# Performance work log

Hardware: AMD Instinct MI355X
Metric: run time of the kernel (lower is better)

Reference implementation:

```python
import jax, jax.numpy as jnp
import numpy as np

# --- config-derived constants (match init_kwargs) ---
BATCH = 16
TEMP = 0.1
N_REGIONS = 9
IMG = 512
NUM_FILTERS = 5      # len(no_filters)-1
N_DEC_BLOCKS = 2
SIZE_FACTOR = 1 << (NUM_FILTERS - N_DEC_BLOCKS)   # 8
IM = IMG // SIZE_FACTOR - 4                        # 60
H = W = IM + 2                                     # 62 (feature map spatial size)
C = 512
EPS = 1e-6

_h = IM // 2  # 30
_X = _Y = IM  # 60
POS = np.array([[0,0],[0,_h],[0,_Y],[_h,0],[_h,_h],[_h,_Y],[_X,0],[_X,_h],[_X,_Y]], np.int32)
NEG = np.array([
  [[0,_h],[_h,0],[_h,_h],[0,_Y],[_X,0]],
  [[0,0],[0,_Y],[_h,0],[_h,_h],[_h,_Y]],
  [[0,0],[0,_h],[_h,_h],[_h,_Y],[_X,_Y]],
  [[0,0],[0,_h],[_h,_h],[_X,0],[_X,_h]],
  [[0,0],[0,_h],[_h,0],[_h,_Y],[_X,_h]],
  [[0,_h],[0,_Y],[_h,_h],[_X,_h],[_X,_Y]],
  [[0,0],[_h,0],[_h,_h],[_X,_h],[_X,_Y]],
  [[_h,0],[_h,_h],[_h,_Y],[_X,0],[_X,_Y]],
  [[0,_Y],[_h,_h],[_h,_Y],[_X,0],[_X,_h]],
], np.int32)

def _patch_flat(idx):
    # idx [..., 2] (row, col) -> flat indices of the 2x2 patch, [..., 4]
    base = idx[..., 0] * W + idx[..., 1]
    return np.stack([base, base + 1, base + W, base + W + 1], axis=-1)

POS_FLAT = jnp.asarray(_patch_flat(POS))     # [9, 4]
NEG_FLAT = jnp.asarray(_patch_flat(NEG))     # [9, 5, 4]

def _cos(a, b):
    # cosine similarity over last axis, torch-style eps clamp on the norm product
    dot = jnp.sum(a * b, axis=-1)
    na = jnp.sqrt(jnp.sum(a * a, axis=-1))
    nb = jnp.sqrt(jnp.sum(b * b, axis=-1))
    return dot / jnp.maximum(na * nb, EPS)


def setup_inputs() -> dict:
    key = jax.random.key(0)
    x = jax.random.normal(key, (BATCH, C, H, W), dtype=jnp.float32)
    return {"x": x}


def reference(x):
    B = x.shape[0]
    xf = x.reshape(B, C, H * W)
    pp = xf[:, :, POS_FLAT]   # [B, C, 9, 4]
    nn_ = xf[:, :, NEG_FLAT]  # [B, C, 9, 5, 4]
    i1p, i2p = pp[0::2], pp[1::2]      # [P, C, 9, 4]
    i1n, i2n = nn_[0::2], nn_[1::2]    # [P, C, 9, 5, 4]

    # positive similarity (symmetric: cos(i1,i2) == cos(i2,i1))
    num_ss = _cos(i1p, i2p) / TEMP                 # [P, C, 9]
    S = jnp.sum(jnp.exp(num_ss), axis=1)           # [P, 9]

    a1 = i1p[:, :, :, None, :]                     # [P, C, 9, 1, 4]
    a2 = i2p[:, :, :, None, :]
    den1 = jnp.exp(_cos(a1, i1n) / TEMP) + jnp.exp(_cos(a1, i2n) / TEMP)  # [P, C, 9, 5]
    den2 = jnp.exp(_cos(a2, i2n) / TEMP) + jnp.exp(_cos(a2, i1n) / TEMP)
    D1 = jnp.sum(den1, axis=(1, 3))                # [P, 9]
    D2 = jnp.sum(den2, axis=(1, 3))

    loss = jnp.sum(-jnp.log(S / (S + D1)) - jnp.log(S / (S + D2)))
    return loss / B / N_REGIONS
```

## Files before the change

### kernel.cpp

```cpp
#include <hip/hip_runtime.h>
#include <math.h>

#define NPAIR 8
#define NREG 9
#define NCH 512
#define HW 3844
#define W62 62
#define NPATCH 9

__constant__ int PATCH_BASE[9] = {0, 30, 60, 1860, 1890, 1920, 3720, 3750, 3780};
__constant__ int NEG_IDX[9][5] = {
    {1, 3, 4, 2, 6},
    {0, 2, 3, 4, 5},
    {0, 1, 4, 5, 8},
    {0, 1, 4, 6, 7},
    {0, 1, 3, 5, 7},
    {1, 2, 4, 7, 8},
    {0, 3, 4, 7, 8},
    {3, 4, 5, 6, 8},
    {2, 4, 5, 6, 7}};

__device__ __forceinline__ float dot4(const float4& a, const float4& b) {
    return a.x * b.x + a.y * b.y + a.z * b.z + a.w * b.w;
}

__device__ __forceinline__ float wave_sum(float v) {
    #pragma unroll
    for (int off = 32; off > 0; off >>= 1) v += __shfl_down(v, off, 64);
    return v;
}

__global__ __launch_bounds__(256) void lcl_gather(const float* __restrict__ x,
                                                  float4* __restrict__ g,
                                                  float* __restrict__ out) {
    const int tid = blockIdx.x * 256 + threadIdx.x;
    if (tid == 0) out[0] = 0.0f;
    const int c = tid & (NCH - 1);
    const int bp = tid >> 9;
    const int patch = bp % NPATCH;
    const int b = bp / NPATCH;
    const float* src = x + (size_t)(b * NCH + c) * HW + PATCH_BASE[patch];
    const float2 a0 = *(const float2*)(src);
    const float2 a1 = *(const float2*)(src + W62);
    g[(size_t)bp * NCH + c] = make_float4(a0.x, a0.y, a1.x, a1.y);
}

__global__ __launch_bounds__(512) void lcl_partial(const float4* __restrict__ g,
                                                   float* __restrict__ out) {
    const int blk = blockIdx.x;
    const int p = blk / NREG;
    const int r = blk % NREG;
    const int c = threadIdx.x;

    const float4* g1 = g + (size_t)(2 * p) * NPATCH * NCH + c;
    const float4* g2 = g + (size_t)(2 * p + 1) * NPATCH * NCH + c;

    const float4 v1 = g1[r * NCH];
    const float4 v2 = g2[r * NCH];
    const float nv1 = dot4(v1, v1);
    const float nv2 = dot4(v2, v2);

    float s = expf(10.0f * dot4(v1, v2) / fmaxf(sqrtf(nv1 * nv2), 1e-6f));
    float d1 = 0.0f, d2 = 0.0f;
    #pragma unroll
    for (int j = 0; j < 5; j++) {
        const int q = NEG_IDX[r][j];
        const float4 n1 = g1[q * NCH];
        const float4 n2 = g2[q * NCH];
        const float nn1 = dot4(n1, n1);
        const float nn2 = dot4(n2, n2);
        d1 += expf(10.0f * dot4(v1, n1) / fmaxf(sqrtf(nv1 * nn1), 1e-6f));
        d1 += expf(10.0f * dot4(v1, n2) / fmaxf(sqrtf(nv1 * nn2), 1e-6f));
        d2 += expf(10.0f * dot4(v2, n2) / fmaxf(sqrtf(nv2 * nn2), 1e-6f));
        d2 += expf(10.0f * dot4(v2, n1) / fmaxf(sqrtf(nv2 * nn1), 1e-6f));
    }

    s = wave_sum(s);
    d1 = wave_sum(d1);
    d2 = wave_sum(d2);

    __shared__ float sm[3][8];
    const int wave = threadIdx.x >> 6;
    const int lane = threadIdx.x & 63;
    if (lane == 0) { sm[0][wave] = s; sm[1][wave] = d1; sm[2][wave] = d2; }
    __syncthreads();
    if (threadIdx.x == 0) {
        float S = 0.0f, D1 = 0.0f, D2 = 0.0f;
        #pragma unroll
        for (int w = 0; w < 8; w++) { S += sm[0][w]; D1 += sm[1][w]; D2 += sm[2][w]; }
        const float term = logf(S + D1) + logf(S + D2) - 2.0f * logf(S);
        atomicAdd(out, term * (1.0f / 144.0f));
    }
}

extern "C" void kernel_launch(void* const* d_in, const int* in_sizes, int n_in,
                              void* d_out, int out_size, void* d_ws, size_t ws_size,
                              hipStream_t stream) {
    const float* x = (const float*)d_in[0];
    float* out = (float*)d_out;
    float4* g = (float4*)d_ws;

    lcl_gather<<<(16 * NPATCH * NCH) / 256, 256, 0, stream>>>(x, g, out);
    lcl_partial<<<NPAIR * NREG, 512, 0, stream>>>(g, out);
}
```

Before: 159.0 us.

## Fuse gather into main kernel and finish reduction with cooperative grid sync

Drops the separate gather kernel and its workspace round-trip: each block now loads its 2x2 patches straight from the input. The per-block atomicAdd is replaced by writing per-block terms to workspace, then a cooperative grid sync lets block 0 do a deterministic final sum. If the cooperative launch fails, the code falls back to a plain launch followed by a small final kernel. The direct loads are strided 8-byte reads, and cooperative launch may carry its own launch overhead.

```diff
diff --git a/kernel.cpp b/kernel.cpp
--- a/kernel.cpp
+++ b/kernel.cpp
@@ -1,5 +1,8 @@
 #include <hip/hip_runtime.h>
+#include <hip/hip_cooperative_groups.h>
 #include <math.h>
+
+namespace cg = cooperative_groups;
 
 #define NPAIR 8
 #define NREG 9
@@ -7,6 +10,7 @@
 #define HW 3844
 #define W62 62
 #define NPATCH 9
+#define NBLK (NPAIR * NREG)
 
 __constant__ int PATCH_BASE[9] = {0, 30, 60, 1860, 1890, 1920, 3720, 3750, 3780};
 __constant__ int NEG_IDX[9][5] = {
@@ -30,49 +34,46 @@
     return v;
 }
 
-__global__ __launch_bounds__(256) void lcl_gather(const float* __restrict__ x,
-                                                  float4* __restrict__ g,
-                                                  float* __restrict__ out) {
-    const int tid = blockIdx.x * 256 + threadIdx.x;
-    if (tid == 0) out[0] = 0.0f;
-    const int c = tid & (NCH - 1);
-    const int bp = tid >> 9;
-    const int patch = bp % NPATCH;
-    const int b = bp / NPATCH;
-    const float* src = x + (size_t)(b * NCH + c) * HW + PATCH_BASE[patch];
-    const float2 a0 = *(const float2*)(src);
-    const float2 a1 = *(const float2*)(src + W62);
-    g[(size_t)bp * NCH + c] = make_float4(a0.x, a0.y, a1.x, a1.y);
+__device__ __forceinline__ float4 ld_patch(const float* p) {
+    const float2 a0 = *(const float2*)(p);
+    const float2 a1 = *(const float2*)(p + W62);
+    return make_float4(a0.x, a0.y, a1.x, a1.y);
 }
 
-__global__ __launch_bounds__(512) void lcl_partial(const float4* __restrict__ g,
-                                                   float* __restrict__ out) {
+template <bool COOP>
+__global__ __launch_bounds__(512) void lcl_main(const float* __restrict__ x,
+                                                float* __restrict__ ws,
+                                                float* __restrict__ out) {
     const int blk = blockIdx.x;
     const int p = blk / NREG;
     const int r = blk % NREG;
     const int c = threadIdx.x;
 
-    const float4* g1 = g + (size_t)(2 * p) * NPATCH * NCH + c;
-    const float4* g2 = g + (size_t)(2 * p + 1) * NPATCH * NCH + c;
+    const float* x1 = x + (size_t)(2 * p * NCH + c) * HW;
+    const float* x2 = x + (size_t)((2 * p + 1) * NCH + c) * HW;
 
-    const float4 v1 = g1[r * NCH];
-    const float4 v2 = g2[r * NCH];
+    const float4 v1 = ld_patch(x1 + PATCH_BASE[r]);
+    const float4 v2 = ld_patch(x2 + PATCH_BASE[r]);
+    float4 n1[5], n2[5];
+    #pragma unroll
+    for (int j = 0; j < 5; j++) {
+        const int q = PATCH_BASE[NEG_IDX[r][j]];
+        n1[j] = ld_patch(x1 + q);
+        n2[j] = ld_patch(x2 + q);
+    }
+
     const float nv1 = dot4(v1, v1);
     const float nv2 = dot4(v2, v2);
-
     float s = expf(10.0f * dot4(v1, v2) / fmaxf(sqrtf(nv1 * nv2), 1e-6f));
     float d1 = 0.0f, d2 = 0.0f;
     #pragma unroll
     for (int j = 0; j < 5; j++) {
-        const int q = NEG_IDX[r][j];
-        const float4 n1 = g1[q * NCH];
-        const float4 n2 = g2[q * NCH];
-        const float nn1 = dot4(n1, n1);
-        const float nn2 = dot4(n2, n2);
-        d1 += expf(10.0f * dot4(v1, n1) / fmaxf(sqrtf(nv1 * nn1), 1e-6f));
-        d1 += expf(10.0f * dot4(v1, n2) / fmaxf(sqrtf(nv1 * nn2), 1e-6f));
-        d2 += expf(10.0f * dot4(v2, n2) / fmaxf(sqrtf(nv2 * nn2), 1e-6f));
-        d2 += expf(10.0f * dot4(v2, n1) / fmaxf(sqrtf(nv2 * nn1), 1e-6f));
+        const float nn1 = dot4(n1[j], n1[j]);
+        const float nn2 = dot4(n2[j], n2[j]);
+        d1 += expf(10.0f * dot4(v1, n1[j]) / fmaxf(sqrtf(nv1 * nn1), 1e-6f));
+        d1 += expf(10.0f * dot4(v1, n2[j]) / fmaxf(sqrtf(nv1 * nn2), 1e-6f));
+        d2 += expf(10.0f * dot4(v2, n2[j]) / fmaxf(sqrtf(nv2 * nn2), 1e-6f));
+        d2 += expf(10.0f * dot4(v2, n1[j]) / fmaxf(sqrtf(nv2 * nn1), 1e-6f));
     }
 
     s = wave_sum(s);
@@ -88,9 +89,27 @@
         float S = 0.0f, D1 = 0.0f, D2 = 0.0f;
         #pragma unroll
         for (int w = 0; w < 8; w++) { S += sm[0][w]; D1 += sm[1][w]; D2 += sm[2][w]; }
-        const float term = logf(S + D1) + logf(S + D2) - 2.0f * logf(S);
-        atomicAdd(out, term * (1.0f / 144.0f));
+        ws[blk] = logf(S + D1) + logf(S + D2) - 2.0f * logf(S);
+        __threadfence();
     }
+
+    if constexpr (COOP) {
+        cg::this_grid().sync();
+        if (blk == 0 && threadIdx.x < 64) {
+            float t = ws[threadIdx.x];
+            if (threadIdx.x < 8) t += ws[64 + threadIdx.x];
+            t = wave_sum(t);
+            if (threadIdx.x == 0) out[0] = t * (1.0f / 144.0f);
+        }
+    }
+}
+
+__global__ __launch_bounds__(64) void lcl_final(const float* __restrict__ ws,
+                                                float* __restrict__ out) {
+    float t = ws[threadIdx.x];
+    if (threadIdx.x < 8) t += ws[64 + threadIdx.x];
+    t = wave_sum(t);
+    if (threadIdx.x == 0) out[0] = t * (1.0f / 144.0f);
 }
 
 extern "C" void kernel_launch(void* const* d_in, const int* in_sizes, int n_in,
@@ -98,8 +117,14 @@
                               hipStream_t stream) {
     const float* x = (const float*)d_in[0];
     float* out = (float*)d_out;
-    float4* g = (float4*)d_ws;
+    float* ws = (float*)d_ws;
 
-    lcl_gather<<<(16 * NPATCH * NCH) / 256, 256, 0, stream>>>(x, g, out);
-    lcl_partial<<<NPAIR * NREG, 512, 0, stream>>>(g, out);
+    void* args[] = {(void*)&x, (void*)&ws, (void*)&out};
+    hipError_t e = hipLaunchCooperativeKernel(
+        reinterpret_cast<void*>(lcl_main<true>), dim3(NBLK), dim3(512), args, 0,
+        stream);
+    if (e != hipSuccess) {
+        lcl_main<false><<<NBLK, 512, 0, stream>>>(x, ws, out);
+        lcl_final<<<1, 64, 0, stream>>>(ws, out);
+    }
 }
```

Result: slower. 196.8 us (+23.8%).
